# Kernel tuning notes

Measured on AMD Instinct MI355X. Metric: run time of the kernel, lower is better.

Reference implementation:

```python
import jax, jax.numpy as jnp
import numpy as np

B, T, E = 1, 4096, 1024
H = 16
D = E // H  # head_dim = 64


def setup_inputs() -> dict:
    key = jax.random.key(0)
    k1, k2, k3 = jax.random.split(key, 3)
    x = jax.random.normal(k1, (B, T, E), dtype=jnp.float32)
    w_qkv = jax.random.normal(k2, (E, 3 * E), dtype=jnp.float32) * (1.0 / np.sqrt(E))
    b_qkv = jnp.zeros((3 * E,), dtype=jnp.float32)
    w_out = jax.random.normal(k3, (E, E), dtype=jnp.float32) * (1.0 / np.sqrt(E))
    b_out = jnp.zeros((E,), dtype=jnp.float32)
    return {"x": x, "w_qkv": w_qkv, "b_qkv": b_qkv, "w_out": w_out, "b_out": b_out}


def reference(x, w_qkv, b_qkv, w_out, b_out):
    b, t, e = x.shape
    scale = 1.0 / np.sqrt(D)
    qkv = x @ w_qkv + b_qkv                      # [b, t, 3e]
    q, k, v = jnp.split(qkv, 3, axis=-1)
    # [b, h, t, d]
    q = q.reshape(b, t, H, D).transpose(0, 2, 1, 3)
    k = k.reshape(b, t, H, D).transpose(0, 2, 1, 3)
    v = v.reshape(b, t, H, D).transpose(0, 2, 1, 3)
    attn = jnp.einsum("bhqd,bhkd->bhqk", q, k) * scale  # [b, h, t, t]
    causal = jnp.tril(jnp.ones((t, t), dtype=bool))
    attn = jnp.where(causal, attn, -jnp.inf)
    attn = jax.nn.softmax(attn, axis=-1)
    out = jnp.einsum("bhqk,bhkd->bhqd", attn, v)        # [b, h, t, d]
    out = out.transpose(0, 2, 1, 3).reshape(b, t, e)
    return out @ w_out + b_out
```

## Files before the change

kernel.cpp:

```cpp
#include <hip/hip_runtime.h>
#include <hip/hip_bf16.h>


#define T_SEQ 4096
#define EMB   1024
#define NH    16
#define HD    64
#define N_QKV 3072

typedef __bf16 bf16x8 __attribute__((ext_vector_type(8)));
typedef __bf16 bf16x4 __attribute__((ext_vector_type(4)));
typedef float  f32x4  __attribute__((ext_vector_type(4)));

__device__ inline f32x4 mfma16(bf16x8 a, bf16x8 b, f32x4 c) {
    return __builtin_amdgcn_mfma_f32_16x16x32_bf16(a, b, c, 0, 0, 0);
}

__device__ inline void async_copy16(const void* g, void* l) {
    __builtin_amdgcn_global_load_lds(
        (const __attribute__((address_space(1))) unsigned int*)g,
        (__attribute__((address_space(3))) unsigned int*)l, 16, 0, 0);
}

__device__ inline bf16x8 lds_read8(const __bf16* base, int row, int colByte) {
    return *(const bf16x8*)((const char*)base + row * 128 +
                            (colByte ^ ((row & 7) << 4)));
}

__global__ __launch_bounds__(256) void prep_kernel(const float* __restrict__ x,
                                                   const float* __restrict__ w_qkv,
                                                   const float* __restrict__ w_out,
                                                   __bf16* __restrict__ xb,
                                                   __bf16* __restrict__ wqkvT,
                                                   __bf16* __restrict__ woutT) {
    __shared__ __bf16 tl[32][33];
    int b = blockIdx.x;
    int t = threadIdx.x;
    if (b < 4096) {
        int i = (b * 256 + t) * 4;
        float4 v = *(const float4*)&x[i];
        bf16x4 o;
        o[0] = (__bf16)v.x; o[1] = (__bf16)v.y; o[2] = (__bf16)v.z; o[3] = (__bf16)v.w;
        *(bf16x4*)&xb[i] = o;
        return;
    }
    const float* in;
    __bf16* out;
    int N, bb;
    if (b < 7168) { bb = b - 4096; in = w_qkv; out = wqkvT; N = N_QKV; }
    else          { bb = b - 7168; in = w_out; out = woutT; N = EMB; }
    int k0 = (bb & 31) * 32, n0 = (bb >> 5) * 32;
    int r = t >> 3, c4 = (t & 7) * 4;
    float4 v = *(const float4*)&in[(size_t)(k0 + r) * N + n0 + c4];
    tl[r][c4 + 0] = (__bf16)v.x;
    tl[r][c4 + 1] = (__bf16)v.y;
    tl[r][c4 + 2] = (__bf16)v.z;
    tl[r][c4 + 3] = (__bf16)v.w;
    __syncthreads();
    bf16x4 o;
    o[0] = tl[c4 + 0][r];
    o[1] = tl[c4 + 1][r];
    o[2] = tl[c4 + 2][r];
    o[3] = tl[c4 + 3][r];
    *(bf16x4*)&out[(size_t)(n0 + r) * EMB + k0 + c4] = o;
}

__global__ __launch_bounds__(256) void gemm_qkv_kernel(const __bf16* __restrict__ A,
                                                       const __bf16* __restrict__ Bt,
                                                       const float* __restrict__ bias,
                                                       __bf16* __restrict__ Qo,
                                                       __bf16* __restrict__ Ko,
                                                       __bf16* __restrict__ Vo) {
    const int K = EMB;
    int m0 = blockIdx.y * 128, n0 = blockIdx.x * 128;
    int tid = threadIdx.x;
    int w = tid >> 6, l = tid & 63, lg = l >> 4, lr = l & 15;
    int wr = w >> 1, wc = w & 1;

    __shared__ __align__(16) __bf16 As[128 * 32];
    __shared__ __align__(16) __bf16 Bs[128 * 32];

    f32x4 acc[4][4];
#pragma unroll
    for (int mi = 0; mi < 4; ++mi)
#pragma unroll
        for (int ni = 0; ni < 4; ++ni) acc[mi][ni] = (f32x4){0.f, 0.f, 0.f, 0.f};

    for (int k0 = 0; k0 < K; k0 += 32) {
        __syncthreads();
#pragma unroll
        for (int i = 0; i < 2; ++i) {
            int flat = tid + 256 * i;
            int row = flat >> 2, c = flat & 3;
            async_copy16(&A[(size_t)(m0 + row) * K + k0 + c * 8], As + flat * 8);
            async_copy16(&Bt[(size_t)(n0 + row) * K + k0 + c * 8], Bs + flat * 8);
        }
        __syncthreads();
        bf16x8 af[4], bfr[4];
#pragma unroll
        for (int mi = 0; mi < 4; ++mi) af[mi] = *(const bf16x8*)(As + (wr * 64 + mi * 16 + lr) * 32 + lg * 8);
#pragma unroll
        for (int ni = 0; ni < 4; ++ni) bfr[ni] = *(const bf16x8*)(Bs + (wc * 64 + ni * 16 + lr) * 32 + lg * 8);
#pragma unroll
        for (int mi = 0; mi < 4; ++mi)
#pragma unroll
            for (int ni = 0; ni < 4; ++ni)
                acc[mi][ni] = mfma16(af[mi], bfr[ni], acc[mi][ni]);
    }

    const float QSC = 0.18033688011112042f;
#pragma unroll
    for (int mi = 0; mi < 4; ++mi) {
#pragma unroll
        for (int ni = 0; ni < 4; ++ni) {
            int n = n0 + wc * 64 + ni * 16 + lr;
            float bv = bias[n];
            int mat = n >> 10, rem = n & 1023, hh = rem >> 6, d = rem & 63;
#pragma unroll
            for (int r = 0; r < 4; ++r) {
                int mr = m0 + wr * 64 + mi * 16 + lg * 4 + r;
                float v = acc[mi][ni][r] + bv;
                size_t idx = ((size_t)hh * T_SEQ + mr) * HD + d;
                if (mat == 0)      Qo[idx] = (__bf16)(v * QSC);
                else if (mat == 1) Ko[idx] = (__bf16)v;
                else               Vo[idx] = (__bf16)v;
            }
        }
    }
}

__global__ __launch_bounds__(256) void vt_kernel(const __bf16* __restrict__ V,
                                                 __bf16* __restrict__ VT) {
    __shared__ __bf16 tl[64][72];
    int h = blockIdx.y, t0 = blockIdx.x * 64;
    int tid = threadIdx.x;
    const __bf16* Vh = V + (size_t)h * T_SEQ * HD;
#pragma unroll
    for (int i = 0; i < 2; ++i) {
        int flat = tid + 256 * i;
        int r = flat >> 3, sl = flat & 7;
        *(bf16x8*)&tl[r][sl * 8] = *(const bf16x8*)&Vh[(size_t)(t0 + r) * HD + sl * 8];
    }
    __syncthreads();
    __bf16* VTh = VT + (size_t)h * HD * T_SEQ;
#pragma unroll
    for (int i = 0; i < 2; ++i) {
        int flat = tid + 256 * i;
        int d = flat >> 3, sl = flat & 7;
        bf16x8 o;
#pragma unroll
        for (int j = 0; j < 8; ++j) o[j] = tl[sl * 8 + j][d];
        *(bf16x8*)&VTh[(size_t)d * T_SEQ + t0 + sl * 8] = o;
    }
}

__global__ __launch_bounds__(256) void attn_kernel(const __bf16* __restrict__ Qg,
                                                   const __bf16* __restrict__ Kg,
                                                   const __bf16* __restrict__ VTg,
                                                   __bf16* __restrict__ Og) {
    __shared__ __align__(16) __bf16 Ks[2][64 * 64];
    __shared__ __align__(16) __bf16 Vs[2][64 * 64];
    __shared__ __align__(16) __bf16 Ps[4][16 * 64];

    const int bid = blockIdx.x;
    const int xcd = bid & 7, li = bid >> 3;
    const int h = xcd * 2 + (li & 1);
    const int pr = li >> 1;
    const int tid = threadIdx.x;
    const int w = tid >> 6, l = tid & 63, lg = l >> 4, lr = l & 15;

    const __bf16* Qh = Qg + (size_t)h * T_SEQ * HD;
    const __bf16* Kh = Kg + (size_t)h * T_SEQ * HD;
    const __bf16* Vh = VTg + (size_t)h * HD * T_SEQ;
    __bf16* PsW = &Ps[w][0];

    const int srow = tid >> 3, sslot = tid & 7;
    const int sB = (sslot * 16) ^ ((srow & 7) << 4);
    const size_t kOff0 = (size_t)srow * HD + (sB >> 1);
    const size_t kOff1 = kOff0 + (size_t)32 * HD;
    const size_t vOff0 = (size_t)srow * T_SEQ + (sB >> 1);
    const size_t vOff1 = vOff0 + (size_t)32 * T_SEQ;

#pragma unroll 1
    for (int ph = 0; ph < 2; ++ph) {
        const int bx = ph ? pr : (63 - pr);
        const int qr0 = bx * 64 + 16 * w;

        bf16x8 qf[2];
#pragma unroll
        for (int kd = 0; kd < 2; ++kd)
            qf[kd] = *(const bf16x8*)&Qh[(size_t)(qr0 + lr) * HD + kd * 32 + lg * 8];

        f32x4 oacc[4];
#pragma unroll
        for (int n = 0; n < 4; ++n) oacc[n] = (f32x4){0.f, 0.f, 0.f, 0.f};
        float m = -1e30f, lsum = 0.f;

        const int ntiles = bx + 1;

        async_copy16(Kh + kOff0, &Ks[0][tid * 8]);
        async_copy16(Kh + kOff1, &Ks[0][(tid + 256) * 8]);
        async_copy16(Vh + vOff0, &Vs[0][tid * 8]);
        async_copy16(Vh + vOff1, &Vs[0][(tid + 256) * 8]);
        __syncthreads();

        int cur = 0;
        for (int t = 0; t < ntiles; ++t) {
            const int kv0 = t * 64;
            if (t + 1 < ntiles) {
                const size_t kb = (size_t)(t + 1) * 64 * HD;
                const size_t vb = (size_t)(t + 1) * 64;
                async_copy16(Kh + kb + kOff0, &Ks[cur ^ 1][tid * 8]);
                async_copy16(Kh + kb + kOff1, &Ks[cur ^ 1][(tid + 256) * 8]);
                async_copy16(Vh + vb + vOff0, &Vs[cur ^ 1][tid * 8]);
                async_copy16(Vh + vb + vOff1, &Vs[cur ^ 1][(tid + 256) * 8]);
            }
            const __bf16* Ksc = &Ks[cur][0];
            const __bf16* Vsc = &Vs[cur][0];

            bf16x8 kf[4][2];
#pragma unroll
            for (int blk = 0; blk < 4; ++blk)
#pragma unroll
                for (int kd = 0; kd < 2; ++kd)
                    kf[blk][kd] = lds_read8(Ksc, blk * 16 + lr, kd * 64 + lg * 16);

            __builtin_amdgcn_s_setprio(1);
            f32x4 s[4];
#pragma unroll
            for (int blk = 0; blk < 4; ++blk) {
                f32x4 a = (f32x4){0.f, 0.f, 0.f, 0.f};
                a = mfma16(kf[blk][0], qf[0], a);
                a = mfma16(kf[blk][1], qf[1], a);
                s[blk] = a;
            }
            __builtin_amdgcn_s_setprio(0);

            float mx = -1e30f;
            if (kv0 + 63 > qr0) {
#pragma unroll
                for (int blk = 0; blk < 4; ++blk)
#pragma unroll
                    for (int r = 0; r < 4; ++r) {
                        int kv = kv0 + 16 * blk + 4 * lg + r;
                        float sv = (kv <= qr0 + lr) ? s[blk][r] : -1e30f;
                        s[blk][r] = sv;
                        mx = fmaxf(mx, sv);
                    }
            } else {
#pragma unroll
                for (int blk = 0; blk < 4; ++blk)
#pragma unroll
                    for (int r = 0; r < 4; ++r) mx = fmaxf(mx, s[blk][r]);
            }

            if (!__all(mx <= m + 8.f)) {
                float mf = fmaxf(mx, __shfl_xor(mx, 16, 64));
                mf = fmaxf(mf, __shfl_xor(mf, 32, 64));
                float mnew = fmaxf(m, mf);
                float alpha = exp2f(m - mnew);
                m = mnew;
                lsum *= alpha;
                float ar[4];
#pragma unroll
                for (int r = 0; r < 4; ++r) ar[r] = __shfl(alpha, 4 * lg + r, 64);
#pragma unroll
                for (int n = 0; n < 4; ++n)
#pragma unroll
                    for (int r = 0; r < 4; ++r) oacc[n][r] *= ar[r];
            }

            float ps = 0.f;
            char* pw = (char*)PsW + lr * 128;
            const int swz = (lr & 7) << 4;
#pragma unroll
            for (int blk = 0; blk < 4; ++blk) {
                bf16x4 pk;
#pragma unroll
                for (int r = 0; r < 4; ++r) {
                    float p = exp2f(s[blk][r] - m);
                    ps += p;
                    pk[r] = (__bf16)p;
                }
                *(bf16x4*)(pw + ((32 * blk + 8 * lg) ^ swz)) = pk;
            }
            lsum += ps;

            __builtin_amdgcn_s_setprio(1);
#pragma unroll
            for (int kc = 0; kc < 2; ++kc) {
                bf16x8 pa = lds_read8(PsW, lr, kc * 64 + lg * 16);
#pragma unroll
                for (int n = 0; n < 4; ++n) {
                    bf16x8 vb = lds_read8(Vsc, 16 * n + lr, kc * 64 + lg * 16);
                    oacc[n] = mfma16(pa, vb, oacc[n]);
                }
            }
            __builtin_amdgcn_s_setprio(0);

            __syncthreads();
            cur ^= 1;
        }

        lsum += __shfl_xor(lsum, 16, 64);
        lsum += __shfl_xor(lsum, 32, 64);
        float linv = 1.0f / lsum;
        float lrv[4];
#pragma unroll
        for (int r = 0; r < 4; ++r) lrv[r] = __shfl(linv, 4 * lg + r, 64);
#pragma unroll
        for (int n = 0; n < 4; ++n)
#pragma unroll
            for (int r = 0; r < 4; ++r) {
                int q = qr0 + 4 * lg + r;
                Og[(size_t)q * EMB + h * HD + 16 * n + lr] = (__bf16)(oacc[n][r] * lrv[r]);
            }
    }
}

__global__ __launch_bounds__(256) void gemm_out_kernel(const __bf16* __restrict__ A,
                                                       const __bf16* __restrict__ Bt,
                                                       const float* __restrict__ bias,
                                                       float* __restrict__ out) {
    const int K = EMB;
    int m0 = blockIdx.y * 128, n0 = blockIdx.x * 128;
    int tid = threadIdx.x;
    int w = tid >> 6, l = tid & 63, lg = l >> 4, lr = l & 15;
    int wr = w >> 1, wc = w & 1;

    __shared__ __align__(16) __bf16 As[128 * 32];
    __shared__ __align__(16) __bf16 Bs[128 * 32];

    f32x4 acc[4][4];
#pragma unroll
    for (int mi = 0; mi < 4; ++mi)
#pragma unroll
        for (int ni = 0; ni < 4; ++ni) acc[mi][ni] = (f32x4){0.f, 0.f, 0.f, 0.f};

    for (int k0 = 0; k0 < K; k0 += 32) {
        __syncthreads();
#pragma unroll
        for (int i = 0; i < 2; ++i) {
            int flat = tid + 256 * i;
            int row = flat >> 2, c = flat & 3;
            async_copy16(&A[(size_t)(m0 + row) * K + k0 + c * 8], As + flat * 8);
            async_copy16(&Bt[(size_t)(n0 + row) * K + k0 + c * 8], Bs + flat * 8);
        }
        __syncthreads();
        bf16x8 af[4], bfr[4];
#pragma unroll
        for (int mi = 0; mi < 4; ++mi) af[mi] = *(const bf16x8*)(As + (wr * 64 + mi * 16 + lr) * 32 + lg * 8);
#pragma unroll
        for (int ni = 0; ni < 4; ++ni) bfr[ni] = *(const bf16x8*)(Bs + (wc * 64 + ni * 16 + lr) * 32 + lg * 8);
#pragma unroll
        for (int mi = 0; mi < 4; ++mi)
#pragma unroll
            for (int ni = 0; ni < 4; ++ni)
                acc[mi][ni] = mfma16(af[mi], bfr[ni], acc[mi][ni]);
    }

#pragma unroll
    for (int mi = 0; mi < 4; ++mi) {
#pragma unroll
        for (int ni = 0; ni < 4; ++ni) {
            int n = n0 + wc * 64 + ni * 16 + lr;
            float bv = bias[n];
#pragma unroll
            for (int r = 0; r < 4; ++r) {
                int mr = m0 + wr * 64 + mi * 16 + lg * 4 + r;
                out[(size_t)mr * EMB + n] = acc[mi][ni][r] + bv;
            }
        }
    }
}

extern "C" void kernel_launch(void* const* d_in, const int* in_sizes, int n_in,
                              void* d_out, int out_size, void* d_ws, size_t ws_size,
                              hipStream_t stream) {
    const float* x      = (const float*)d_in[0];
    const float* w_qkv  = (const float*)d_in[1];
    const float* b_qkv  = (const float*)d_in[2];
    const float* w_out  = (const float*)d_in[3];
    const float* b_out  = (const float*)d_in[4];
    float* out = (float*)d_out;

    char* ws = (char*)d_ws;
    __bf16* xb    = (__bf16*)(ws);
    __bf16* AO    = (__bf16*)(ws);
    __bf16* wqkvT = (__bf16*)(ws + ((size_t)8 << 20));
    __bf16* woutT = (__bf16*)(ws + ((size_t)14 << 20));
    __bf16* Qh    = (__bf16*)(ws + ((size_t)16 << 20));
    __bf16* Kh    = (__bf16*)(ws + ((size_t)24 << 20));
    __bf16* Vh    = (__bf16*)(ws + ((size_t)32 << 20));
    __bf16* VTh   = (__bf16*)(ws + ((size_t)40 << 20));

    prep_kernel<<<dim3(8192), 256, 0, stream>>>(x, w_qkv, w_out, xb, wqkvT, woutT);

    gemm_qkv_kernel<<<dim3(N_QKV / 128, T_SEQ / 128), 256, 0, stream>>>(xb, wqkvT, b_qkv, Qh, Kh, Vh);

    vt_kernel<<<dim3(T_SEQ / 64, NH), 256, 0, stream>>>(Vh, VTh);

    attn_kernel<<<dim3(512), 256, 0, stream>>>(Qh, Kh, VTh, AO);

    gemm_out_kernel<<<dim3(EMB / 128, T_SEQ / 128), 256, 0, stream>>>(AO, woutT, b_out, out);
}
```

Measured before the change: 227.0 us.

## Use 512-thread attention blocks with 128-row query tiles and unrolled double buffering

The attention kernel now runs 8 waves per block over a 128-row query tile, so each K/V tile loaded into LDS is shared by twice as many query rows. The old two-phase pairing of short and long causal rows inside one block is replaced by a block-index ordering that schedules long tiles first. The KV loop is unrolled by two with fixed buffer indices and precomputed LDS addresses, and waves whose rows lie entirely before a tile skip it. The cost is that the waves of a block become imbalanced on the diagonal tiles, and the larger block with launch_bounds(512,4) may add register pressure.

```diff
diff --git a/kernel.cpp b/kernel.cpp
--- a/kernel.cpp
+++ b/kernel.cpp
@@ -154,168 +154,166 @@
     }
 }
 
-__global__ __launch_bounds__(256) void attn_kernel(const __bf16* __restrict__ Qg,
-                                                   const __bf16* __restrict__ Kg,
-                                                   const __bf16* __restrict__ VTg,
-                                                   __bf16* __restrict__ Og) {
+__global__ __launch_bounds__(512, 4) void attn_kernel(const __bf16* __restrict__ Qg,
+                                                      const __bf16* __restrict__ Kg,
+                                                      const __bf16* __restrict__ VTg,
+                                                      __bf16* __restrict__ Og) {
     __shared__ __align__(16) __bf16 Ks[2][64 * 64];
     __shared__ __align__(16) __bf16 Vs[2][64 * 64];
-    __shared__ __align__(16) __bf16 Ps[4][16 * 64];
+    __shared__ __align__(16) __bf16 Ps[8][16 * 64];
 
     const int bid = blockIdx.x;
-    const int xcd = bid & 7, li = bid >> 3;
-    const int h = xcd * 2 + (li & 1);
-    const int pr = li >> 1;
+    const int h = bid & 15;
+    const int i = bid >> 4;
+    const int bx = (i < 16) ? (31 - i) : (i - 16);
     const int tid = threadIdx.x;
     const int w = tid >> 6, l = tid & 63, lg = l >> 4, lr = l & 15;
+    const int qr0 = bx * 128 + 16 * w;
 
     const __bf16* Qh = Qg + (size_t)h * T_SEQ * HD;
     const __bf16* Kh = Kg + (size_t)h * T_SEQ * HD;
     const __bf16* Vh = VTg + (size_t)h * HD * T_SEQ;
-    __bf16* PsW = &Ps[w][0];
 
     const int srow = tid >> 3, sslot = tid & 7;
     const int sB = (sslot * 16) ^ ((srow & 7) << 4);
-    const size_t kOff0 = (size_t)srow * HD + (sB >> 1);
-    const size_t kOff1 = kOff0 + (size_t)32 * HD;
-    const size_t vOff0 = (size_t)srow * T_SEQ + (sB >> 1);
-    const size_t vOff1 = vOff0 + (size_t)32 * T_SEQ;
-
-#pragma unroll 1
-    for (int ph = 0; ph < 2; ++ph) {
-        const int bx = ph ? pr : (63 - pr);
-        const int qr0 = bx * 64 + 16 * w;
-
-        bf16x8 qf[2];
-#pragma unroll
-        for (int kd = 0; kd < 2; ++kd)
-            qf[kd] = *(const bf16x8*)&Qh[(size_t)(qr0 + lr) * HD + kd * 32 + lg * 8];
-
-        f32x4 oacc[4];
-#pragma unroll
-        for (int n = 0; n < 4; ++n) oacc[n] = (f32x4){0.f, 0.f, 0.f, 0.f};
-        float m = -1e30f, lsum = 0.f;
-
-        const int ntiles = bx + 1;
-
-        async_copy16(Kh + kOff0, &Ks[0][tid * 8]);
-        async_copy16(Kh + kOff1, &Ks[0][(tid + 256) * 8]);
-        async_copy16(Vh + vOff0, &Vs[0][tid * 8]);
-        async_copy16(Vh + vOff1, &Vs[0][(tid + 256) * 8]);
-        __syncthreads();
-
-        int cur = 0;
-        for (int t = 0; t < ntiles; ++t) {
-            const int kv0 = t * 64;
-            if (t + 1 < ntiles) {
-                const size_t kb = (size_t)(t + 1) * 64 * HD;
-                const size_t vb = (size_t)(t + 1) * 64;
-                async_copy16(Kh + kb + kOff0, &Ks[cur ^ 1][tid * 8]);
-                async_copy16(Kh + kb + kOff1, &Ks[cur ^ 1][(tid + 256) * 8]);
-                async_copy16(Vh + vb + vOff0, &Vs[cur ^ 1][tid * 8]);
-                async_copy16(Vh + vb + vOff1, &Vs[cur ^ 1][(tid + 256) * 8]);
-            }
-            const __bf16* Ksc = &Ks[cur][0];
-            const __bf16* Vsc = &Vs[cur][0];
-
-            bf16x8 kf[4][2];
-#pragma unroll
-            for (int blk = 0; blk < 4; ++blk)
-#pragma unroll
-                for (int kd = 0; kd < 2; ++kd)
-                    kf[blk][kd] = lds_read8(Ksc, blk * 16 + lr, kd * 64 + lg * 16);
-
-            __builtin_amdgcn_s_setprio(1);
-            f32x4 s[4];
-#pragma unroll
-            for (int blk = 0; blk < 4; ++blk) {
-                f32x4 a = (f32x4){0.f, 0.f, 0.f, 0.f};
-                a = mfma16(kf[blk][0], qf[0], a);
-                a = mfma16(kf[blk][1], qf[1], a);
-                s[blk] = a;
-            }
-            __builtin_amdgcn_s_setprio(0);
-
-            float mx = -1e30f;
-            if (kv0 + 63 > qr0) {
-#pragma unroll
-                for (int blk = 0; blk < 4; ++blk)
-#pragma unroll
-                    for (int r = 0; r < 4; ++r) {
-                        int kv = kv0 + 16 * blk + 4 * lg + r;
-                        float sv = (kv <= qr0 + lr) ? s[blk][r] : -1e30f;
-                        s[blk][r] = sv;
-                        mx = fmaxf(mx, sv);
-                    }
-            } else {
-#pragma unroll
-                for (int blk = 0; blk < 4; ++blk)
-#pragma unroll
-                    for (int r = 0; r < 4; ++r) mx = fmaxf(mx, s[blk][r]);
-            }
-
-            if (!__all(mx <= m + 8.f)) {
-                float mf = fmaxf(mx, __shfl_xor(mx, 16, 64));
-                mf = fmaxf(mf, __shfl_xor(mf, 32, 64));
-                float mnew = fmaxf(m, mf);
-                float alpha = exp2f(m - mnew);
-                m = mnew;
-                lsum *= alpha;
-                float ar[4];
-#pragma unroll
-                for (int r = 0; r < 4; ++r) ar[r] = __shfl(alpha, 4 * lg + r, 64);
-#pragma unroll
-                for (int n = 0; n < 4; ++n)
-#pragma unroll
-                    for (int r = 0; r < 4; ++r) oacc[n][r] *= ar[r];
-            }
-
-            float ps = 0.f;
-            char* pw = (char*)PsW + lr * 128;
-            const int swz = (lr & 7) << 4;
-#pragma unroll
-            for (int blk = 0; blk < 4; ++blk) {
-                bf16x4 pk;
-#pragma unroll
-                for (int r = 0; r < 4; ++r) {
-                    float p = exp2f(s[blk][r] - m);
-                    ps += p;
-                    pk[r] = (__bf16)p;
-                }
-                *(bf16x4*)(pw + ((32 * blk + 8 * lg) ^ swz)) = pk;
-            }
-            lsum += ps;
-
-            __builtin_amdgcn_s_setprio(1);
-#pragma unroll
-            for (int kc = 0; kc < 2; ++kc) {
-                bf16x8 pa = lds_read8(PsW, lr, kc * 64 + lg * 16);
-#pragma unroll
-                for (int n = 0; n < 4; ++n) {
-                    bf16x8 vb = lds_read8(Vsc, 16 * n + lr, kc * 64 + lg * 16);
-                    oacc[n] = mfma16(pa, vb, oacc[n]);
-                }
-            }
-            __builtin_amdgcn_s_setprio(0);
-
-            __syncthreads();
-            cur ^= 1;
+    const __bf16* kSrc = Kh + (size_t)srow * HD + (sB >> 1);
+    const __bf16* vSrc = Vh + (size_t)srow * T_SEQ + (sB >> 1);
+
+    const int coff0 = (lg * 16) ^ ((lr & 7) << 4);
+    const int coff1 = coff0 ^ 64;
+    const char* KB0 = (const char*)Ks + lr * 128 + coff0;
+    const char* KB1 = (const char*)Ks + lr * 128 + coff1;
+    const char* VB0 = (const char*)Vs + lr * 128 + coff0;
+    const char* VB1 = (const char*)Vs + lr * 128 + coff1;
+    char* PW = (char*)Ps + w * 2048 + lr * 128;
+    const char* PA0 = PW + coff0;
+    const char* PA1 = PW + coff1;
+    char* pwr0 = PW + ((0  + 8 * lg) ^ ((lr & 7) << 4));
+    char* pwr1 = PW + ((32 + 8 * lg) ^ ((lr & 7) << 4));
+    char* pwr2 = PW + ((64 + 8 * lg) ^ ((lr & 7) << 4));
+    char* pwr3 = PW + ((96 + 8 * lg) ^ ((lr & 7) << 4));
+
+    bf16x8 qf[2];
+#pragma unroll
+    for (int kd = 0; kd < 2; ++kd)
+        qf[kd] = *(const bf16x8*)&Qh[(size_t)(qr0 + lr) * HD + kd * 32 + lg * 8];
+
+    f32x4 oacc[4];
+#pragma unroll
+    for (int n = 0; n < 4; ++n) oacc[n] = (f32x4){0.f, 0.f, 0.f, 0.f};
+    float m = -1e30f, lsum = 0.f;
+
+    const int ntiles = 2 * bx + 2;
+
+#define ATTN_STAGE(BUF)                                          \
+    do {                                                         \
+        async_copy16(kSrc, &Ks[BUF][tid * 8]);                   \
+        async_copy16(vSrc, &Vs[BUF][tid * 8]);                   \
+        kSrc += 64 * HD;                                         \
+        vSrc += 64;                                              \
+    } while (0)
+
+#define ATTN_TILE(BUF, KV0)                                                       \
+    if ((KV0) <= qr0 + 15) {                                                      \
+        bf16x8 kf[4][2];                                                          \
+        _Pragma("unroll") for (int blk = 0; blk < 4; ++blk) {                     \
+            kf[blk][0] = *(const bf16x8*)(KB0 + (BUF) * 8192 + blk * 2048);       \
+            kf[blk][1] = *(const bf16x8*)(KB1 + (BUF) * 8192 + blk * 2048);       \
+        }                                                                         \
+        __builtin_amdgcn_s_setprio(1);                                            \
+        f32x4 s[4];                                                               \
+        _Pragma("unroll") for (int blk = 0; blk < 4; ++blk) {                     \
+            f32x4 a = (f32x4){0.f, 0.f, 0.f, 0.f};                                \
+            a = mfma16(kf[blk][0], qf[0], a);                                     \
+            a = mfma16(kf[blk][1], qf[1], a);                                     \
+            s[blk] = a;                                                           \
+        }                                                                         \
+        __builtin_amdgcn_s_setprio(0);                                            \
+        float mx = -1e30f;                                                        \
+        if ((KV0) + 63 > qr0) {                                                   \
+            _Pragma("unroll") for (int blk = 0; blk < 4; ++blk)                   \
+                _Pragma("unroll") for (int r = 0; r < 4; ++r) {                   \
+                    int kv = (KV0) + 16 * blk + 4 * lg + r;                       \
+                    float sv = (kv <= qr0 + lr) ? s[blk][r] : -1e30f;             \
+                    s[blk][r] = sv;                                               \
+                    mx = fmaxf(mx, sv);                                           \
+                }                                                                 \
+        } else {                                                                  \
+            _Pragma("unroll") for (int blk = 0; blk < 4; ++blk)                   \
+                _Pragma("unroll") for (int r = 0; r < 4; ++r)                     \
+                    mx = fmaxf(mx, s[blk][r]);                                    \
+        }                                                                         \
+        if (!__all(mx <= m + 8.f)) {                                              \
+            float mf = fmaxf(mx, __shfl_xor(mx, 16, 64));                         \
+            mf = fmaxf(mf, __shfl_xor(mf, 32, 64));                               \
+            float mnew = fmaxf(m, mf);                                            \
+            float alpha = exp2f(m - mnew);                                        \
+            m = mnew;                                                             \
+            lsum *= alpha;                                                        \
+            float ar[4];                                                          \
+            _Pragma("unroll") for (int r = 0; r < 4; ++r)                         \
+                ar[r] = __shfl(alpha, 4 * lg + r, 64);                            \
+            _Pragma("unroll") for (int n = 0; n < 4; ++n)                         \
+                _Pragma("unroll") for (int r = 0; r < 4; ++r)                     \
+                    oacc[n][r] *= ar[r];                                          \
+        }                                                                         \
+        {                                                                         \
+            float ps = 0.f;                                                       \
+            bf16x4 pk0, pk1, pk2, pk3;                                            \
+            _Pragma("unroll") for (int r = 0; r < 4; ++r) {                       \
+                float p0 = exp2f(s[0][r] - m); ps += p0; pk0[r] = (__bf16)p0;     \
+                float p1 = exp2f(s[1][r] - m); ps += p1; pk1[r] = (__bf16)p1;     \
+                float p2 = exp2f(s[2][r] - m); ps += p2; pk2[r] = (__bf16)p2;     \
+                float p3 = exp2f(s[3][r] - m); ps += p3; pk3[r] = (__bf16)p3;     \
+            }                                                                     \
+            *(bf16x4*)pwr0 = pk0;                                                 \
+            *(bf16x4*)pwr1 = pk1;                                                 \
+            *(bf16x4*)pwr2 = pk2;                                                 \
+            *(bf16x4*)pwr3 = pk3;                                                 \
+            lsum += ps;                                                           \
+        }                                                                         \
+        {                                                                         \
+            bf16x8 pa0 = *(const bf16x8*)PA0;                                     \
+            bf16x8 pa1 = *(const bf16x8*)PA1;                                     \
+            __builtin_amdgcn_s_setprio(1);                                        \
+            _Pragma("unroll") for (int n = 0; n < 4; ++n) {                       \
+                bf16x8 vb0 = *(const bf16x8*)(VB0 + (BUF) * 8192 + n * 2048);     \
+                bf16x8 vb1 = *(const bf16x8*)(VB1 + (BUF) * 8192 + n * 2048);     \
+                oacc[n] = mfma16(pa0, vb0, oacc[n]);                              \
+                oacc[n] = mfma16(pa1, vb1, oacc[n]);                              \
+            }                                                                     \
+            __builtin_amdgcn_s_setprio(0);                                        \
+        }                                                                         \
+    }
+
+    ATTN_STAGE(0);
+    __syncthreads();
+
+    for (int t = 0; t < ntiles; t += 2) {
+        ATTN_STAGE(1);
+        ATTN_TILE(0, t * 64)
+        __syncthreads();
+        if (t + 2 < ntiles) ATTN_STAGE(0);
+        ATTN_TILE(1, (t + 1) * 64)
+        __syncthreads();
+    }
+
+#undef ATTN_STAGE
+#undef ATTN_TILE
+
+    lsum += __shfl_xor(lsum, 16, 64);
+    lsum += __shfl_xor(lsum, 32, 64);
+    float linv = 1.0f / lsum;
+    float lrv[4];
+#pragma unroll
+    for (int r = 0; r < 4; ++r) lrv[r] = __shfl(linv, 4 * lg + r, 64);
+#pragma unroll
+    for (int n = 0; n < 4; ++n)
+#pragma unroll
+        for (int r = 0; r < 4; ++r) {
+            int q = qr0 + 4 * lg + r;
+            Og[(size_t)q * EMB + h * HD + 16 * n + lr] = (__bf16)(oacc[n][r] * lrv[r]);
         }
-
-        lsum += __shfl_xor(lsum, 16, 64);
-        lsum += __shfl_xor(lsum, 32, 64);
-        float linv = 1.0f / lsum;
-        float lrv[4];
-#pragma unroll
-        for (int r = 0; r < 4; ++r) lrv[r] = __shfl(linv, 4 * lg + r, 64);
-#pragma unroll
-        for (int n = 0; n < 4; ++n)
-#pragma unroll
-            for (int r = 0; r < 4; ++r) {
-                int q = qr0 + 4 * lg + r;
-                Og[(size_t)q * EMB + h * HD + 16 * n + lr] = (__bf16)(oacc[n][r] * lrv[r]);
-            }
-    }
 }
 
 __global__ __launch_bounds__(256) void gemm_out_kernel(const __bf16* __restrict__ A,
@@ -400,7 +398,7 @@
 
     vt_kernel<<<dim3(T_SEQ / 64, NH), 256, 0, stream>>>(Vh, VTh);
 
-    attn_kernel<<<dim3(512), 256, 0, stream>>>(Qh, Kh, VTh, AO);
+    attn_kernel<<<dim3(512), 512, 0, stream>>>(Qh, Kh, VTh, AO);
 
     gemm_out_kernel<<<dim3(EMB / 128, T_SEQ / 128), 256, 0, stream>>>(AO, woutT, b_out, out);
 }
```

New measurement: 224.9 us. About the same (-0.9%).
